# Kernel optimization log

Measured on AMD Instinct MI355X. Metric: run time of the kernel, lower is better.

## Reference

```python
import jax, jax.numpy as jnp
import numpy as np

B, S, W = 16, 256, 128            # batch, seq_len (word pieces), words per sentence
V, H, L, NH, DH, FF, C = 30522, 768, 12, 12, 64, 3072, 425
EPS = 1e-12                        # HF Bert LayerNorm eps


def setup_inputs() -> dict:
    key = jax.random.key(0)
    kiter = iter(jax.random.split(key, 64))
    nk = lambda: next(kiter)
    # each word maps to 1 or 2 word-pieces -> total pieces in [W, 2W] <= S
    word_piece_tracked = jax.random.randint(nk(), (B, W), 1, 3)
    lengths = jnp.sum(word_piece_tracked, axis=1)
    encoded_batch = jax.random.randint(nk(), (B, S), 0, V)
    mask = (jnp.arange(S)[None, :] < lengths[:, None]).astype(jnp.int32)
    p = lambda *shape: jax.random.normal(nk(), shape, jnp.float32) * 0.02
    return dict(
        encoded_batch=encoded_batch, mask=mask, word_piece_tracked=word_piece_tracked,
        word_emb=p(V, H), pos_emb=p(S, H), type_emb=p(1, H),
        emb_ln_s=jnp.ones((H,), jnp.float32), emb_ln_b=jnp.zeros((H,), jnp.float32),
        Wq=p(L, H, H), bq=p(L, H), Wk=p(L, H, H), bk=p(L, H),
        Wv=p(L, H, H), bv=p(L, H), Wo=p(L, H, H), bo=p(L, H),
        ln1_s=jnp.ones((L, H), jnp.float32), ln1_b=jnp.zeros((L, H), jnp.float32),
        Wi=p(L, H, FF), bi=p(L, FF), Wo2=p(L, FF, H), bo2=p(L, H),
        ln2_s=jnp.ones((L, H), jnp.float32), ln2_b=jnp.zeros((L, H), jnp.float32),
        w1=p(H, 1024), b1=p(1024), w2=p(1024, C), b2=p(C),
    )


def _layer_norm(x, s, b):
    mu = jnp.mean(x, -1, keepdims=True)
    var = jnp.var(x, -1, keepdims=True)
    return (x - mu) * jax.lax.rsqrt(var + EPS) * s + b


def _forward(encoded_batch, mask, word_piece_tracked,
             word_emb, pos_emb, type_emb, emb_ln_s, emb_ln_b,
             Wq, bq, Wk, bk, Wv, bv, Wo, bo, ln1_s, ln1_b,
             Wi, bi, Wo2, bo2, ln2_s, ln2_b, w1, b1, w2, b2):
    # BERT embeddings (token_type all zeros)
    x = word_emb[encoded_batch] + pos_emb[None, :, :] + type_emb[0]
    x = _layer_norm(x, emb_ln_s, emb_ln_b)
    attn_bias = (1.0 - mask.astype(jnp.float32))[:, None, None, :] * -10000.0
    scale = 1.0 / np.sqrt(DH).astype(np.float32)

    def step(h, lp):
        wq, bq_, wk, bk_, wv, bv_, wo, bo_, l1s, l1b, wi, bi_, wo2, bo2_, l2s, l2b = lp
        q = (h @ wq + bq_).reshape(B, S, NH, DH)
        k = (h @ wk + bk_).reshape(B, S, NH, DH)
        v = (h @ wv + bv_).reshape(B, S, NH, DH)
        att = jax.nn.softmax(jnp.einsum('bqhd,bkhd->bhqk', q, k) * scale + attn_bias, axis=-1)
        ctx = jnp.einsum('bhqk,bkhd->bqhd', att, v).reshape(B, S, H)
        h = _layer_norm(h + ctx @ wo + bo_, l1s, l1b)
        ff = jax.nn.gelu(h @ wi + bi_, approximate=False)
        h = _layer_norm(h + ff @ wo2 + bo2_, l2s, l2b)
        return h, None

    x, _ = jax.lax.scan(step, x, (Wq, bq, Wk, bk, Wv, bv, Wo, bo, ln1_s, ln1_b,
                                  Wi, bi, Wo2, bo2, ln2_s, ln2_b))

    # MLP head (dropout = identity in eval)
    f1 = jax.nn.relu(x) @ w1 + b1          # [B, S, 1024]
    f2 = jax.nn.relu(f1) @ w2 + b2          # [B, S, C]

    # ragged segment-mean pooling over word pieces (equiv. to the python loop)
    cum = jnp.cumsum(word_piece_tracked, axis=1)                         # [B, W]
    seg = jax.vmap(lambda c: jnp.searchsorted(c, jnp.arange(S), side='right'))(cum)  # [B, S]
    sums = jax.vmap(lambda f, s: jax.ops.segment_sum(f, s, num_segments=W))(f2, seg)
    pooled = sums / word_piece_tracked[..., None].astype(f2.dtype)       # [B, W, C]
    out = jnp.concatenate([pooled, f2[:, W:, :]], axis=1)                # [B, S, C]
    return jax.nn.softmax(out, axis=2)


def reference(encoded_batch, mask, word_piece_tracked,
              word_emb, pos_emb, type_emb, emb_ln_s, emb_ln_b,
              Wq, bq, Wk, bk, Wv, bv, Wo, bo, ln1_s, ln1_b,
              Wi, bi, Wo2, bo2, ln2_s, ln2_b, w1, b1, w2, b2):
    return _forward(encoded_batch, mask, word_piece_tracked,
                    word_emb, pos_emb, type_emb, emb_ln_s, emb_ln_b,
                    Wq, bq, Wk, bk, Wv, bv, Wo, bo, ln1_s, ln1_b,
                    Wi, bi, Wo2, bo2, ln2_s, ln2_b, w1, b1, w2, b2)
```

## Files before the change

### kernel.cpp

```cpp
#include <hip/hip_runtime.h>
#include <math.h>

#define BB 16
#define SS 256
#define WW 128
#define HH 768
#define LL 12
#define NHH 12
#define DHH 64
#define FFD 3072
#define CC 425
#define NTOK (BB*SS)
#define QKVN (3*HH)

typedef __attribute__((ext_vector_type(8))) short bf16x8;
typedef __attribute__((ext_vector_type(4))) float f32x4;

__device__ __forceinline__ float bf2f(unsigned short u) {
    union { unsigned int i; float f; } z; z.i = ((unsigned int)u) << 16; return z.f;
}
__device__ __forceinline__ unsigned short f2bf(float f) {
    union { float f; unsigned int i; } z; z.f = f;
    unsigned int i = z.i;
    unsigned int r = (i + 0x7fffu + ((i >> 16) & 1u)) >> 16;
    return (unsigned short)r;
}

__device__ __forceinline__ void gload16(const void* g, void* l) {
    __builtin_amdgcn_global_load_lds((const __attribute__((address_space(1))) void*)g,
                                     (__attribute__((address_space(3))) void*)l, 16, 0, 0);
}

__device__ __forceinline__ float gelu_f(float v) {
    float ax = fabsf(v) * 0.70710678118654752f;
    float t = 1.0f / fmaf(0.3275911f, ax, 1.0f);
    float poly = t * fmaf(t, fmaf(t, fmaf(t, fmaf(t, 1.061405429f, -1.453152027f),
                                          1.421413741f), -0.284496736f), 0.254829592f);
    float er = 1.0f - poly * __expf(-ax * ax);
    er = (v < 0.f) ? -er : er;
    return 0.5f * v * (1.0f + er);
}

__device__ __forceinline__ int xcd_remap(int nwg, int orig) {
    int q = nwg >> 3, r = nwg & 7, xc = orig & 7, o8 = orig >> 3;
    return (xc < r ? xc * (q + 1) : r * (q + 1) + (xc - r) * q) + o8;
}

template<int ACT_C>
__launch_bounds__(512)
__global__ void gemm128(const unsigned short* __restrict__ A,
                        const unsigned short* __restrict__ Bt,
                        const float* __restrict__ bias,
                        unsigned short* __restrict__ Cm,
                        int M, int N, int K, int ldC) {
    constexpr int BUFS = 128 * 32;
    __shared__ __align__(16) unsigned short lA[2 * BUFS];
    __shared__ __align__(16) unsigned short lB[2 * BUFS];
    const int tid = threadIdx.x, w = tid >> 6, l = tid & 63;

    const int gx = gridDim.x;
    const int wg = xcd_remap(gx * gridDim.y, blockIdx.y * gx + blockIdx.x);
    const int m0 = (wg / gx) * 128, n0 = (wg % gx) * 128;

    const int wr = (w >> 2) * 64, wc = (w & 3) * 32;
    const int lr = l & 15, lk = (l >> 4) * 8;
    const int rsw = ((lr >> 1) & 3) << 4;
    const int lrow = l >> 2;
    const int gs = (l & 3) ^ ((lrow >> 1) & 3);

    f32x4 acc[4][2];
#pragma unroll
    for (int m = 0; m < 4; ++m)
#pragma unroll
        for (int n = 0; n < 2; ++n) acc[m][n] = (f32x4){0.f, 0.f, 0.f, 0.f};

    auto stage = [&](int k0, unsigned short* dA, unsigned short* dB) {
        gload16(A + (size_t)(m0 + w * 16 + lrow) * K + k0 + gs * 8, dA + w * 512);
        gload16(Bt + (size_t)(n0 + w * 16 + lrow) * K + k0 + gs * 8, dB + w * 512);
    };

    const int nt = K >> 5;
    stage(0, lA, lB);
    __syncthreads();

    for (int t = 0; t < nt; ++t) {
        unsigned short* cA = lA + (t & 1) * BUFS;
        unsigned short* cB = lB + (t & 1) * BUFS;
        if (t + 1 < nt)
            stage((t + 1) << 5, lA + ((t + 1) & 1) * BUFS, lB + ((t + 1) & 1) * BUFS);
        bf16x8 af[4], bfr[2];
#pragma unroll
        for (int m = 0; m < 4; ++m) {
            int row = wr + m * 16 + lr;
            af[m] = *(const bf16x8*)((const char*)cA + row * 64 + ((lk * 2) ^ rsw));
        }
#pragma unroll
        for (int n = 0; n < 2; ++n) {
            int row = wc + n * 16 + lr;
            bfr[n] = *(const bf16x8*)((const char*)cB + row * 64 + ((lk * 2) ^ rsw));
        }
#pragma unroll
        for (int m = 0; m < 4; ++m)
#pragma unroll
            for (int n = 0; n < 2; ++n)
                acc[m][n] = __builtin_amdgcn_mfma_f32_16x16x32_bf16(af[m], bfr[n], acc[m][n], 0, 0, 0);
        __syncthreads();
    }

    const int orow = (l >> 4) * 4, ocol = l & 15;
#pragma unroll
    for (int m = 0; m < 4; ++m)
#pragma unroll
        for (int n = 0; n < 2; ++n) {
            int c = n0 + wc + n * 16 + ocol;
            if (c >= N) continue;
            float bb = bias[c];
#pragma unroll
            for (int j = 0; j < 4; ++j) {
                int rr = m0 + wr + m * 16 + orow + j;
                float vv = acc[m][n][j] + bb;
                if (ACT_C == 1) vv = gelu_f(vv);
                if (ACT_C == 2) vv = fmaxf(vv, 0.f);
                Cm[(size_t)rr * ldC + c] = f2bf(vv);
            }
        }
}

template<int ACT_C>
__launch_bounds__(256)
__global__ void gemm64(const unsigned short* __restrict__ A,
                       const unsigned short* __restrict__ Bt,
                       const float* __restrict__ bias,
                       unsigned short* __restrict__ Cm,
                       int M, int N, int K, int ldC) {
    constexpr int BUFS = 2 * 64 * 32;
    __shared__ __align__(16) unsigned short lA[2 * BUFS];
    __shared__ __align__(16) unsigned short lB[2 * BUFS];
    const int tid = threadIdx.x, w = tid >> 6, l = tid & 63;

    const int gx = gridDim.x;
    const int wg = xcd_remap(gx * gridDim.y, blockIdx.y * gx + blockIdx.x);
    const int m0 = (wg / gx) * 64, n0 = (wg % gx) * 64;

    const int wr = (w >> 1) * 32, wc = (w & 1) * 32;
    const int lr = l & 15, lk = (l >> 4) * 8;
    const int rsw = ((lr >> 1) & 3) << 4;
    const int lrow = l >> 2;
    const int gs = (l & 3) ^ ((lrow >> 1) & 3);

    f32x4 acc[2][2];
#pragma unroll
    for (int m = 0; m < 2; ++m)
#pragma unroll
        for (int n = 0; n < 2; ++n) acc[m][n] = (f32x4){0.f, 0.f, 0.f, 0.f};

    auto stage = [&](int k0, unsigned short* dA, unsigned short* dB) {
#pragma unroll
        for (int h = 0; h < 2; ++h) {
            gload16(A + (size_t)(m0 + w * 16 + lrow) * K + k0 + h * 32 + gs * 8,
                    dA + h * 2048 + w * 512);
            gload16(Bt + (size_t)(n0 + w * 16 + lrow) * K + k0 + h * 32 + gs * 8,
                    dB + h * 2048 + w * 512);
        }
    };

    const int nt = K >> 6;
    stage(0, lA, lB);
    __syncthreads();

    for (int t = 0; t < nt; ++t) {
        unsigned short* cA = lA + (t & 1) * BUFS;
        unsigned short* cB = lB + (t & 1) * BUFS;
        if (t + 1 < nt)
            stage((t + 1) << 6, lA + ((t + 1) & 1) * BUFS, lB + ((t + 1) & 1) * BUFS);
#pragma unroll
        for (int h = 0; h < 2; ++h) {
            bf16x8 af[2], bfr[2];
#pragma unroll
            for (int m = 0; m < 2; ++m) {
                int row = wr + m * 16 + lr;
                af[m] = *(const bf16x8*)((const char*)cA + h * 4096 + row * 64 + ((lk * 2) ^ rsw));
            }
#pragma unroll
            for (int n = 0; n < 2; ++n) {
                int row = wc + n * 16 + lr;
                bfr[n] = *(const bf16x8*)((const char*)cB + h * 4096 + row * 64 + ((lk * 2) ^ rsw));
            }
#pragma unroll
            for (int m = 0; m < 2; ++m)
#pragma unroll
                for (int n = 0; n < 2; ++n)
                    acc[m][n] = __builtin_amdgcn_mfma_f32_16x16x32_bf16(af[m], bfr[n], acc[m][n], 0, 0, 0);
        }
        __syncthreads();
    }

    const int orow = (l >> 4) * 4, ocol = l & 15;
#pragma unroll
    for (int m = 0; m < 2; ++m)
#pragma unroll
        for (int n = 0; n < 2; ++n) {
            int c = n0 + wc + n * 16 + ocol;
            if (c >= N) continue;
            float bb = bias[c];
#pragma unroll
            for (int j = 0; j < 4; ++j) {
                int rr = m0 + wr + m * 16 + orow + j;
                float vv = acc[m][n][j] + bb;
                if (ACT_C == 1) vv = gelu_f(vv);
                if (ACT_C == 2) vv = fmaxf(vv, 0.f);
                Cm[(size_t)rr * ldC + c] = f2bf(vv);
            }
        }
}

template<int ACT_A, int ACT_C>
__launch_bounds__(256)
__global__ void gemm_aw(const unsigned short* __restrict__ A,
                        const float* __restrict__ Wm,
                        const float* __restrict__ bias,
                        unsigned short* __restrict__ Cm,
                        int M, int N, int K, int ldC) {
    __shared__ __align__(16) unsigned short lA[64][40];
    __shared__ __align__(16) unsigned short lB[64][40];
    const int tid = threadIdx.x;
    const int m0 = blockIdx.y * 64;
    const int n0 = blockIdx.x * 64;
    const int w = tid >> 6, l = tid & 63;
    const int wr = (w >> 1) * 32, wc = (w & 1) * 32;
    const int lr = l & 15, lk = (l >> 4) * 8;

    f32x4 acc[2][2];
#pragma unroll
    for (int m = 0; m < 2; ++m)
#pragma unroll
        for (int n = 0; n < 2; ++n) acc[m][n] = (f32x4){0.f, 0.f, 0.f, 0.f};

    const int arow = tid >> 2, akc = (tid & 3) << 3;
    const int bkr = tid >> 3, bnc = (tid & 7) << 3;
    const bool nvec = (N & 7) == 0;

    for (int k0 = 0; k0 < K; k0 += 32) {
        uint4 av = *(const uint4*)(A + (size_t)(m0 + arow) * K + (k0 + akc));
        if (ACT_A) {
            unsigned short* p = (unsigned short*)&av;
#pragma unroll
            for (int j = 0; j < 8; ++j) if (p[j] & 0x8000u) p[j] = 0;
        }
        *(uint4*)&lA[arow][akc] = av;
        unsigned short bv[8];
        if (nvec) {
            const float* wp = Wm + (size_t)(k0 + bkr) * N + (n0 + bnc);
            float4 w0 = *(const float4*)(wp);
            float4 w1 = *(const float4*)(wp + 4);
            bv[0] = f2bf(w0.x); bv[1] = f2bf(w0.y); bv[2] = f2bf(w0.z); bv[3] = f2bf(w0.w);
            bv[4] = f2bf(w1.x); bv[5] = f2bf(w1.y); bv[6] = f2bf(w1.z); bv[7] = f2bf(w1.w);
        } else {
#pragma unroll
            for (int j = 0; j < 8; ++j) {
                int col = n0 + bnc + j;
                bv[j] = (col < N) ? f2bf(Wm[(size_t)(k0 + bkr) * N + col]) : (unsigned short)0;
            }
        }
#pragma unroll
        for (int j = 0; j < 8; ++j) lB[bnc + j][bkr] = bv[j];
        __syncthreads();

        bf16x8 af[2], bfr[2];
#pragma unroll
        for (int m = 0; m < 2; ++m) af[m] = *(const bf16x8*)&lA[wr + m * 16 + lr][lk];
#pragma unroll
        for (int n = 0; n < 2; ++n) bfr[n] = *(const bf16x8*)&lB[wc + n * 16 + lr][lk];
#pragma unroll
        for (int m = 0; m < 2; ++m)
#pragma unroll
            for (int n = 0; n < 2; ++n)
                acc[m][n] = __builtin_amdgcn_mfma_f32_16x16x32_bf16(af[m], bfr[n], acc[m][n], 0, 0, 0);
        __syncthreads();
    }

    const int orow = (l >> 4) * 4, ocol = l & 15;
#pragma unroll
    for (int m = 0; m < 2; ++m)
#pragma unroll
        for (int n = 0; n < 2; ++n) {
            int c = n0 + wc + n * 16 + ocol;
            if (c >= N) continue;
            float bb = bias[c];
#pragma unroll
            for (int j = 0; j < 4; ++j) {
                int r = m0 + wr + m * 16 + orow + j;
                float vv = acc[m][n][j] + bb;
                if (ACT_C == 1) vv = gelu_f(vv);
                if (ACT_C == 2) vv = fmaxf(vv, 0.f);
                Cm[(size_t)r * ldC + c] = f2bf(vv);
            }
        }
}

__global__ void transpose_w(const float* __restrict__ src, unsigned short* __restrict__ dst,
                            int K, int N, long srcLS, long dstLS) {
    int n0 = blockIdx.x * 32, k0 = blockIdx.y * 32;
    src += (size_t)blockIdx.z * srcLS;
    dst += (size_t)blockIdx.z * dstLS;
    __shared__ float tile[32][33];
    int tx = threadIdx.x & 31, ty = threadIdx.x >> 5;
#pragma unroll
    for (int r = 0; r < 4; ++r) {
        int k = k0 + ty + r * 8, n = n0 + tx;
        tile[ty + r * 8][tx] = (n < N && k < K) ? src[(size_t)k * N + n] : 0.f;
    }
    __syncthreads();
    int col2 = threadIdx.x & 15, rowb = threadIdx.x >> 4;
#pragma unroll
    for (int p = 0; p < 2; ++p) {
        int n = n0 + rowb + p * 16;
        unsigned int lo = f2bf(tile[col2 * 2][rowb + p * 16]);
        unsigned int hi = f2bf(tile[col2 * 2 + 1][rowb + p * 16]);
        *(unsigned int*)(dst + (size_t)n * K + k0 + col2 * 2) = lo | (hi << 16);
    }
}

__global__ void concat_bias(const float* bq, const float* bk, const float* bv, float* bqkv) {
    int i = blockIdx.x * 256 + threadIdx.x;
    if (i >= LL * QKVN) return;
    int lyr = i / QKVN, c = i % QKVN;
    float v = (c < HH) ? bq[lyr * HH + c] : (c < 2 * HH) ? bk[lyr * HH + c - HH] : bv[lyr * HH + c - 2 * HH];
    bqkv[i] = v;
}

__global__ void build_maskbias(const int* mask, float* mb) {
    int i = blockIdx.x * 256 + threadIdx.x;
    mb[i] = mask[i] ? 0.0f : -10000.0f;
}

__launch_bounds__(256)
__global__ void attention_mfma(const unsigned short* __restrict__ qkv,
                               const float* __restrict__ mb,
                               unsigned short* __restrict__ ctx) {
    const int qt = blockIdx.x, h = blockIdx.y, b = blockIdx.z;
    const int tid = threadIdx.x, w = tid >> 6, l = tid & 63;
    __shared__ __align__(16) unsigned short lK[SS * DHH];
    __shared__ __align__(16) unsigned short lVt[DHH * SS];
    const size_t tokbase = (size_t)b * SS * QKVN;

    {
        const unsigned short* kp = qkv + tokbase + (size_t)tid * QKVN + HH + h * DHH;
        const unsigned short* vp = kp + HH;
#pragma unroll
        for (int c = 0; c < 8; ++c) {
            uint4 kd = *(const uint4*)(kp + c * 8);
            *(uint4*)((char*)lK + ((tid * 128 + c * 16) ^ ((tid & 7) << 4))) = kd;
            uint4 vd = *(const uint4*)(vp + c * 8);
            const unsigned short* e = (const unsigned short*)&vd;
#pragma unroll
            for (int j = 0; j < 8; ++j) {
                int d = c * 8 + j;
                *(unsigned short*)((char*)lVt + ((d * 512 + tid * 2) ^ ((d & 7) << 4))) = e[j];
            }
        }
    }
    const int q0w = qt * 64 + w * 16;
    const unsigned short* qp = qkv + tokbase + (size_t)(q0w + (l & 15)) * QKVN + h * DHH + (l >> 4) * 8;
    bf16x8 aq0 = *(const bf16x8*)(qp);
    bf16x8 aq1 = *(const bf16x8*)(qp + 32);
    __syncthreads();

    f32x4 sc[16];
#pragma unroll
    for (int t = 0; t < 16; ++t) {
        int key = t * 16 + (l & 15);
        int base = key * 128;
        int sw = (key & 7) << 4;
        bf16x8 bk0 = *(const bf16x8*)((char*)lK + ((base + (l >> 4) * 16) ^ sw));
        bf16x8 bk1 = *(const bf16x8*)((char*)lK + ((base + 64 + (l >> 4) * 16) ^ sw));
        f32x4 a = (f32x4){0.f, 0.f, 0.f, 0.f};
        a = __builtin_amdgcn_mfma_f32_16x16x32_bf16(aq0, bk0, a, 0, 0, 0);
        a = __builtin_amdgcn_mfma_f32_16x16x32_bf16(aq1, bk1, a, 0, 0, 0);
        sc[t] = a;
    }
    const float* mbb = mb + b * SS;
    float mx[4] = {-3.0e38f, -3.0e38f, -3.0e38f, -3.0e38f};
#pragma unroll
    for (int t = 0; t < 16; ++t) {
        float mv = mbb[t * 16 + (l & 15)];
#pragma unroll
        for (int r = 0; r < 4; ++r) {
            float v = sc[t][r] * 0.125f + mv;
            sc[t][r] = v;
            mx[r] = fmaxf(mx[r], v);
        }
    }
#pragma unroll
    for (int m = 1; m <= 8; m <<= 1)
#pragma unroll
        for (int r = 0; r < 4; ++r) mx[r] = fmaxf(mx[r], __shfl_xor(mx[r], m));
    float sm[4] = {0.f, 0.f, 0.f, 0.f};
#pragma unroll
    for (int t = 0; t < 16; ++t)
#pragma unroll
        for (int r = 0; r < 4; ++r) {
            float e = __expf(sc[t][r] - mx[r]);
            sc[t][r] = e;
            sm[r] += e;
        }
#pragma unroll
    for (int m = 1; m <= 8; m <<= 1)
#pragma unroll
        for (int r = 0; r < 4; ++r) sm[r] += __shfl_xor(sm[r], m);
    float inv[4];
#pragma unroll
    for (int r = 0; r < 4; ++r) inv[r] = 1.0f / sm[r];

    __syncthreads();
    unsigned short* P = lK;
#pragma unroll
    for (int t = 0; t < 16; ++t)
#pragma unroll
        for (int r = 0; r < 4; ++r) {
            int prow = w * 16 + (l >> 4) * 4 + r;
            int pcol = t * 16 + (l & 15);
            *(unsigned short*)((char*)P + ((prow * 512 + pcol * 2) ^ ((prow & 7) << 4))) =
                f2bf(sc[t][r] * inv[r]);
        }
    __syncthreads();

    f32x4 o[4];
#pragma unroll
    for (int dt = 0; dt < 4; ++dt) o[dt] = (f32x4){0.f, 0.f, 0.f, 0.f};
#pragma unroll
    for (int kt = 0; kt < 8; ++kt) {
        int prow = w * 16 + (l & 15);
        int pkb = (kt * 32 + (l >> 4) * 8) * 2;
        bf16x8 pa = *(const bf16x8*)((char*)P + ((prow * 512 + pkb) ^ ((prow & 7) << 4)));
#pragma unroll
        for (int dt = 0; dt < 4; ++dt) {
            int d = dt * 16 + (l & 15);
            bf16x8 vb = *(const bf16x8*)((char*)lVt + ((d * 512 + pkb) ^ ((d & 7) << 4)));
            o[dt] = __builtin_amdgcn_mfma_f32_16x16x32_bf16(pa, vb, o[dt], 0, 0, 0);
        }
    }
#pragma unroll
    for (int dt = 0; dt < 4; ++dt)
#pragma unroll
        for (int r = 0; r < 4; ++r) {
            int q = qt * 64 + w * 16 + (l >> 4) * 4 + r;
            int d = dt * 16 + (l & 15);
            ctx[((size_t)(b * SS + q)) * HH + h * DHH + d] = f2bf(o[dt][r]);
        }
}

__global__ void embed_ln(const int* __restrict__ ids,
                         const float* __restrict__ we,
                         const float* __restrict__ pe,
                         const float* __restrict__ te,
                         const float* __restrict__ g,
                         const float* __restrict__ beta,
                         unsigned short* __restrict__ x) {
    int t = blockIdx.x, s = t % SS, tid = threadIdx.x;
    int id = ids[t];
    __shared__ float r1[256], r2[256];
    float e[3]; float sum = 0.f, sq = 0.f;
#pragma unroll
    for (int j = 0; j < 3; ++j) {
        int i = tid + j * 256;
        float v = we[(size_t)id * HH + i] + pe[(size_t)s * HH + i] + te[i];
        e[j] = v; sum += v; sq += v * v;
    }
    r1[tid] = sum; r2[tid] = sq; __syncthreads();
    for (int o = 128; o > 0; o >>= 1) {
        if (tid < o) { r1[tid] += r1[tid + o]; r2[tid] += r2[tid + o]; }
        __syncthreads();
    }
    float mu = r1[0] * (1.0f / HH);
    float var = fmaxf(r2[0] * (1.0f / HH) - mu * mu, 0.f);
    float rs = rsqrtf(var + 1e-12f);
#pragma unroll
    for (int j = 0; j < 3; ++j) {
        int i = tid + j * 256;
        x[(size_t)t * HH + i] = f2bf((e[j] - mu) * rs * g[i] + beta[i]);
    }
}

template<int WRITE_RELU>
__launch_bounds__(256)
__global__ void add_ln(unsigned short* __restrict__ x,
                       const unsigned short* __restrict__ y,
                       const float* __restrict__ g,
                       const float* __restrict__ beta,
                       unsigned short* __restrict__ xr) {
    const int t = blockIdx.x * 4 + (threadIdx.x >> 6);
    const int l = threadIdx.x & 63;
    const size_t base = (size_t)t * HH;
    float v[12];
    float sum = 0.f, sq = 0.f;
#pragma unroll
    for (int j = 0; j < 3; ++j) {
        uint2 xa = *(const uint2*)(x + base + j * 256 + l * 4);
        uint2 ya = *(const uint2*)(y + base + j * 256 + l * 4);
        const unsigned short* xp = (const unsigned short*)&xa;
        const unsigned short* yp = (const unsigned short*)&ya;
#pragma unroll
        for (int e = 0; e < 4; ++e) {
            float vv = bf2f(xp[e]) + bf2f(yp[e]);
            v[j * 4 + e] = vv;
            sum += vv; sq += vv * vv;
        }
    }
#pragma unroll
    for (int m = 1; m < 64; m <<= 1) {
        sum += __shfl_xor(sum, m);
        sq += __shfl_xor(sq, m);
    }
    float mu = sum * (1.0f / HH);
    float var = fmaxf(sq * (1.0f / HH) - mu * mu, 0.f);
    float rs = rsqrtf(var + 1e-12f);
#pragma unroll
    for (int j = 0; j < 3; ++j) {
        float4 gg = *(const float4*)(g + j * 256 + l * 4);
        float4 bb = *(const float4*)(beta + j * 256 + l * 4);
        float r0 = (v[j * 4 + 0] - mu) * rs * gg.x + bb.x;
        float r1 = (v[j * 4 + 1] - mu) * rs * gg.y + bb.y;
        float r2 = (v[j * 4 + 2] - mu) * rs * gg.z + bb.z;
        float r3 = (v[j * 4 + 3] - mu) * rs * gg.w + bb.w;
        uint2 st = {(unsigned)f2bf(r0) | ((unsigned)f2bf(r1) << 16),
                    (unsigned)f2bf(r2) | ((unsigned)f2bf(r3) << 16)};
        *(uint2*)(x + base + j * 256 + l * 4) = st;
        if (WRITE_RELU) {
            uint2 sr = {(unsigned)f2bf(fmaxf(r0, 0.f)) | ((unsigned)f2bf(fmaxf(r1, 0.f)) << 16),
                        (unsigned)f2bf(fmaxf(r2, 0.f)) | ((unsigned)f2bf(fmaxf(r3, 0.f)) << 16)};
            *(uint2*)(xr + base + j * 256 + l * 4) = sr;
        }
    }
}

__global__ void cumsum_k(const int* __restrict__ wpt, int* __restrict__ cum) {
    int b = blockIdx.x, w = threadIdx.x;
    int s = 0;
    for (int j = 0; j <= w; ++j) s += wpt[b * WW + j];
    cum[b * WW + w] = s;
}

__global__ void pool_softmax(const unsigned short* __restrict__ f2,
                             const int* __restrict__ cum,
                             float* __restrict__ out) {
    int t = blockIdx.x, b = t / SS, s = t % SS, tid = threadIdx.x;
    __shared__ float red[512];
    float val = -1e30f;
    bool act = tid < CC;
    if (act) {
        if (s < WW) {
            int end = cum[b * WW + s];
            int start = s ? cum[b * WW + s - 1] : 0;
            float su = 0.f;
            for (int j = start; j < end; ++j) su += bf2f(f2[((size_t)b * SS + j) * CC + tid]);
            val = su / (float)(end - start);
        } else {
            val = bf2f(f2[((size_t)b * SS + s) * CC + tid]);
        }
    }
    red[tid] = val; __syncthreads();
    for (int o = 256; o > 0; o >>= 1) {
        if (tid < o) red[tid] = fmaxf(red[tid], red[tid + o]);
        __syncthreads();
    }
    float mx = red[0]; __syncthreads();
    float e = act ? expf(val - mx) : 0.f;
    red[tid] = e; __syncthreads();
    for (int o = 256; o > 0; o >>= 1) {
        if (tid < o) red[tid] += red[tid + o];
        __syncthreads();
    }
    float inv = 1.0f / red[0];
    if (act) out[((size_t)b * SS + s) * CC + tid] = e * inv;
}

static inline size_t al256(size_t x) { return (x + 255) & ~(size_t)255; }

extern "C" void kernel_launch(void* const* d_in, const int* in_sizes, int n_in,
                              void* d_out, int out_size, void* d_ws, size_t ws_size,
                              hipStream_t stream) {
    const int* enc   = (const int*)d_in[0];
    const int* mask  = (const int*)d_in[1];
    const int* wpt   = (const int*)d_in[2];
    const float* word_emb = (const float*)d_in[3];
    const float* pos_emb  = (const float*)d_in[4];
    const float* type_emb = (const float*)d_in[5];
    const float* eln_s = (const float*)d_in[6];
    const float* eln_b = (const float*)d_in[7];
    const float* Wq = (const float*)d_in[8];
    const float* bq = (const float*)d_in[9];
    const float* Wk = (const float*)d_in[10];
    const float* bk = (const float*)d_in[11];
    const float* Wv = (const float*)d_in[12];
    const float* bv = (const float*)d_in[13];
    const float* Wo = (const float*)d_in[14];
    const float* bo = (const float*)d_in[15];
    const float* ln1s = (const float*)d_in[16];
    const float* ln1b = (const float*)d_in[17];
    const float* Wi = (const float*)d_in[18];
    const float* bi = (const float*)d_in[19];
    const float* Wo2 = (const float*)d_in[20];
    const float* bo2 = (const float*)d_in[21];
    const float* ln2s = (const float*)d_in[22];
    const float* ln2b = (const float*)d_in[23];
    const float* w1 = (const float*)d_in[24];
    const float* b1 = (const float*)d_in[25];
    const float* w2 = (const float*)d_in[26];
    const float* b2 = (const float*)d_in[27];

    unsigned char* ws = (unsigned char*)d_ws;
    size_t off = 0;
    unsigned short* x    = (unsigned short*)(ws + off); off = al256(off + (size_t)NTOK * HH * 2);
    unsigned short* qkv  = (unsigned short*)(ws + off); off = al256(off + (size_t)NTOK * QKVN * 2);
    unsigned short* ctx  = (unsigned short*)(ws + off); off = al256(off + (size_t)NTOK * HH * 2);
    unsigned short* proj = (unsigned short*)(ws + off); off = al256(off + (size_t)NTOK * HH * 2);
    unsigned short* ff   = (unsigned short*)(ws + off); off = al256(off + (size_t)NTOK * FFD * 2);
    unsigned short* f1   = (unsigned short*)(ws + off); off = al256(off + (size_t)NTOK * 1024 * 2);
    unsigned short* f2   = (unsigned short*)(ws + off); off = al256(off + (size_t)NTOK * CC * 2);
    unsigned short* xr   = (unsigned short*)(ws + off); off = al256(off + (size_t)NTOK * HH * 2);
    float* mb            = (float*)(ws + off);          off = al256(off + (size_t)NTOK * 4);
    int* cum             = (int*)(ws + off);            off = al256(off + (size_t)BB * WW * 4);
    float* bqkv          = (float*)(ws + off);          off = al256(off + (size_t)LL * QKVN * 4);
    size_t offFast = off;
    unsigned short* WqkvT = (unsigned short*)(ws + offFast); offFast = al256(offFast + (size_t)LL * QKVN * HH * 2);
    unsigned short* WoT   = (unsigned short*)(ws + offFast); offFast = al256(offFast + (size_t)LL * HH * HH * 2);
    unsigned short* WiT   = (unsigned short*)(ws + offFast); offFast = al256(offFast + (size_t)LL * FFD * HH * 2);
    unsigned short* Wo2T  = (unsigned short*)(ws + offFast); offFast = al256(offFast + (size_t)LL * HH * FFD * 2);
    unsigned short* w1T   = (unsigned short*)(ws + offFast); offFast = al256(offFast + (size_t)1024 * HH * 2);
    unsigned short* w2T   = (unsigned short*)(ws + offFast); offFast = al256(offFast + (size_t)512 * 1024 * 2);
    const bool fast = (ws_size >= offFast);

    build_maskbias<<<NTOK / 256, 256, 0, stream>>>(mask, mb);
    concat_bias<<<(LL * QKVN + 255) / 256, 256, 0, stream>>>(bq, bk, bv, bqkv);

    if (fast) {
        transpose_w<<<dim3(24, 24, LL), 256, 0, stream>>>(Wq, WqkvT, HH, HH, (long)HH * HH, (long)QKVN * HH);
        transpose_w<<<dim3(24, 24, LL), 256, 0, stream>>>(Wk, WqkvT + (size_t)HH * HH, HH, HH, (long)HH * HH, (long)QKVN * HH);
        transpose_w<<<dim3(24, 24, LL), 256, 0, stream>>>(Wv, WqkvT + (size_t)2 * HH * HH, HH, HH, (long)HH * HH, (long)QKVN * HH);
        transpose_w<<<dim3(24, 24, LL), 256, 0, stream>>>(Wo, WoT, HH, HH, (long)HH * HH, (long)HH * HH);
        transpose_w<<<dim3(96, 24, LL), 256, 0, stream>>>(Wi, WiT, HH, FFD, (long)HH * FFD, (long)FFD * HH);
        transpose_w<<<dim3(24, 96, LL), 256, 0, stream>>>(Wo2, Wo2T, FFD, HH, (long)FFD * HH, (long)HH * FFD);
        transpose_w<<<dim3(32, 24, 1), 256, 0, stream>>>(w1, w1T, HH, 1024, 0, 0);
        transpose_w<<<dim3(16, 32, 1), 256, 0, stream>>>(w2, w2T, 1024, CC, 0, 0);
    }

    embed_ln<<<NTOK, 256, 0, stream>>>(enc, word_emb, pos_emb, type_emb, eln_s, eln_b, x);

    const dim3 gQKV(QKVN / 128, NTOK / 128);
    const dim3 gWo(HH / 64, NTOK / 64);
    const dim3 gFF1(FFD / 128, NTOK / 128);
    const dim3 gFF2(HH / 64, NTOK / 64);
    const dim3 gH1(1024 / 64, NTOK / 64);
    const dim3 gH2(7, NTOK / 64);
    const dim3 gAttn(4, NHH, BB);

    for (int l = 0; l < LL; ++l) {
        if (fast) {
            gemm128<0><<<gQKV, 512, 0, stream>>>(x, WqkvT + (size_t)l * QKVN * HH, bqkv + l * QKVN, qkv, NTOK, QKVN, HH, QKVN);
        } else {
            const dim3 g64(HH / 64, NTOK / 64);
            gemm_aw<0, 0><<<g64, 256, 0, stream>>>(x, Wq + (size_t)l * HH * HH, bq + l * HH, qkv, NTOK, HH, HH, QKVN);
            gemm_aw<0, 0><<<g64, 256, 0, stream>>>(x, Wk + (size_t)l * HH * HH, bk + l * HH, qkv + HH, NTOK, HH, HH, QKVN);
            gemm_aw<0, 0><<<g64, 256, 0, stream>>>(x, Wv + (size_t)l * HH * HH, bv + l * HH, qkv + 2 * HH, NTOK, HH, HH, QKVN);
        }
        attention_mfma<<<gAttn, 256, 0, stream>>>(qkv, mb, ctx);
        if (fast) {
            gemm64<0><<<gWo, 256, 0, stream>>>(ctx, WoT + (size_t)l * HH * HH, bo + l * HH, proj, NTOK, HH, HH, HH);
        } else {
            gemm_aw<0, 0><<<dim3(HH / 64, NTOK / 64), 256, 0, stream>>>(ctx, Wo + (size_t)l * HH * HH, bo + l * HH, proj, NTOK, HH, HH, HH);
        }
        add_ln<0><<<NTOK / 4, 256, 0, stream>>>(x, proj, ln1s + l * HH, ln1b + l * HH, nullptr);
        if (fast) {
            gemm128<1><<<gFF1, 512, 0, stream>>>(x, WiT + (size_t)l * FFD * HH, bi + l * FFD, ff, NTOK, FFD, HH, FFD);
            gemm64<0><<<gFF2, 256, 0, stream>>>(ff, Wo2T + (size_t)l * HH * FFD, bo2 + l * HH, proj, NTOK, HH, FFD, HH);
        } else {
            gemm_aw<0, 1><<<dim3(FFD / 64, NTOK / 64), 256, 0, stream>>>(x, Wi + (size_t)l * HH * FFD, bi + l * FFD, ff, NTOK, FFD, HH, FFD);
            gemm_aw<0, 0><<<dim3(HH / 64, NTOK / 64), 256, 0, stream>>>(ff, Wo2 + (size_t)l * FFD * HH, bo2 + l * HH, proj, NTOK, HH, FFD, HH);
        }
        if (l == LL - 1)
            add_ln<1><<<NTOK / 4, 256, 0, stream>>>(x, proj, ln2s + l * HH, ln2b + l * HH, xr);
        else
            add_ln<0><<<NTOK / 4, 256, 0, stream>>>(x, proj, ln2s + l * HH, ln2b + l * HH, nullptr);
    }

    if (fast) {
        gemm64<2><<<gH1, 256, 0, stream>>>(xr, w1T, b1, f1, NTOK, 1024, HH, 1024);
        gemm64<0><<<gH2, 256, 0, stream>>>(f1, w2T, b2, f2, NTOK, CC, 1024, CC);
    } else {
        gemm_aw<0, 2><<<dim3(1024 / 64, NTOK / 64), 256, 0, stream>>>(xr, w1, b1, f1, NTOK, 1024, HH, 1024);
        gemm_aw<0, 0><<<dim3(7, NTOK / 64), 256, 0, stream>>>(f1, w2, b2, f2, NTOK, CC, 1024, CC);
    }
    cumsum_k<<<BB, WW, 0, stream>>>(wpt, cum);
    pool_softmax<<<NTOK, 512, 0, stream>>>(f2, cum, (float*)d_out);
}
```

Before: 1.997 ms.

## Split-K the FFN down-projection GEMM and reorder prefetch with MFMA priority

Replaces the FF2 GEMM (K=3072, N=768) with a two-way split-K kernel that writes fp32 partials into the reused qkv buffer, followed by a combine kernel that adds the partials and bias and converts to bf16. This doubles the workgroup count for a GEMM with a small output tile grid and long K, at the cost of extra fp32 partial traffic and one more launch per layer. Separately, the 128-tile GEMM now issues the next-stage global loads after reading its LDS fragments and raises wave priority around the MFMA block. The aim is better overlap of loads with matrix math.

```diff
diff --git a/kernel.cpp b/kernel.cpp
--- a/kernel.cpp
+++ b/kernel.cpp
@@ -86,8 +86,6 @@
     for (int t = 0; t < nt; ++t) {
         unsigned short* cA = lA + (t & 1) * BUFS;
         unsigned short* cB = lB + (t & 1) * BUFS;
-        if (t + 1 < nt)
-            stage((t + 1) << 5, lA + ((t + 1) & 1) * BUFS, lB + ((t + 1) & 1) * BUFS);
         bf16x8 af[4], bfr[2];
 #pragma unroll
         for (int m = 0; m < 4; ++m) {
@@ -99,11 +97,15 @@
             int row = wc + n * 16 + lr;
             bfr[n] = *(const bf16x8*)((const char*)cB + row * 64 + ((lk * 2) ^ rsw));
         }
+        if (t + 1 < nt)
+            stage((t + 1) << 5, lA + ((t + 1) & 1) * BUFS, lB + ((t + 1) & 1) * BUFS);
+        __builtin_amdgcn_s_setprio(1);
 #pragma unroll
         for (int m = 0; m < 4; ++m)
 #pragma unroll
             for (int n = 0; n < 2; ++n)
                 acc[m][n] = __builtin_amdgcn_mfma_f32_16x16x32_bf16(af[m], bfr[n], acc[m][n], 0, 0, 0);
+        __builtin_amdgcn_s_setprio(0);
         __syncthreads();
     }
 
@@ -212,6 +214,107 @@
                 Cm[(size_t)rr * ldC + c] = f2bf(vv);
             }
         }
+}
+
+template<int NS>
+__launch_bounds__(256)
+__global__ void gemm64sk(const unsigned short* __restrict__ A,
+                         const unsigned short* __restrict__ Bt,
+                         float* __restrict__ P,
+                         int M, int N, int K) {
+    constexpr int BUFS = 2 * 64 * 32;
+    __shared__ __align__(16) unsigned short lA[2 * BUFS];
+    __shared__ __align__(16) unsigned short lB[2 * BUFS];
+    const int tid = threadIdx.x, w = tid >> 6, l = tid & 63;
+    const int z = blockIdx.z;
+    const int Kc = K / NS;
+    A += z * Kc;
+    Bt += z * Kc;
+    P += (size_t)z * M * N;
+
+    const int gx = gridDim.x;
+    const int wg = xcd_remap(gx * gridDim.y, blockIdx.y * gx + blockIdx.x);
+    const int m0 = (wg / gx) * 64, n0 = (wg % gx) * 64;
+
+    const int wr = (w >> 1) * 32, wc = (w & 1) * 32;
+    const int lr = l & 15, lk = (l >> 4) * 8;
+    const int rsw = ((lr >> 1) & 3) << 4;
+    const int lrow = l >> 2;
+    const int gs = (l & 3) ^ ((lrow >> 1) & 3);
+
+    f32x4 acc[2][2];
+#pragma unroll
+    for (int m = 0; m < 2; ++m)
+#pragma unroll
+        for (int n = 0; n < 2; ++n) acc[m][n] = (f32x4){0.f, 0.f, 0.f, 0.f};
+
+    auto stage = [&](int k0, unsigned short* dA, unsigned short* dB) {
+#pragma unroll
+        for (int h = 0; h < 2; ++h) {
+            gload16(A + (size_t)(m0 + w * 16 + lrow) * K + k0 + h * 32 + gs * 8,
+                    dA + h * 2048 + w * 512);
+            gload16(Bt + (size_t)(n0 + w * 16 + lrow) * K + k0 + h * 32 + gs * 8,
+                    dB + h * 2048 + w * 512);
+        }
+    };
+
+    const int nt = Kc >> 6;
+    stage(0, lA, lB);
+    __syncthreads();
+
+    for (int t = 0; t < nt; ++t) {
+        unsigned short* cA = lA + (t & 1) * BUFS;
+        unsigned short* cB = lB + (t & 1) * BUFS;
+        if (t + 1 < nt)
+            stage((t + 1) << 6, lA + ((t + 1) & 1) * BUFS, lB + ((t + 1) & 1) * BUFS);
+#pragma unroll
+        for (int h = 0; h < 2; ++h) {
+            bf16x8 af[2], bfr[2];
+#pragma unroll
+            for (int m = 0; m < 2; ++m) {
+                int row = wr + m * 16 + lr;
+                af[m] = *(const bf16x8*)((const char*)cA + h * 4096 + row * 64 + ((lk * 2) ^ rsw));
+            }
+#pragma unroll
+            for (int n = 0; n < 2; ++n) {
+                int row = wc + n * 16 + lr;
+                bfr[n] = *(const bf16x8*)((const char*)cB + h * 4096 + row * 64 + ((lk * 2) ^ rsw));
+            }
+#pragma unroll
+            for (int m = 0; m < 2; ++m)
+#pragma unroll
+                for (int n = 0; n < 2; ++n)
+                    acc[m][n] = __builtin_amdgcn_mfma_f32_16x16x32_bf16(af[m], bfr[n], acc[m][n], 0, 0, 0);
+        }
+        __syncthreads();
+    }
+
+    const int orow = (l >> 4) * 4, ocol = l & 15;
+#pragma unroll
+    for (int m = 0; m < 2; ++m)
+#pragma unroll
+        for (int n = 0; n < 2; ++n) {
+            int c = n0 + wc + n * 16 + ocol;
+#pragma unroll
+            for (int j = 0; j < 4; ++j) {
+                int rr = m0 + wr + m * 16 + orow + j;
+                P[(size_t)rr * N + c] = acc[m][n][j];
+            }
+        }
+}
+
+__global__ void combine2(const float* __restrict__ P, const float* __restrict__ bias,
+                         unsigned short* __restrict__ C, int MN, int N) {
+    int i = blockIdx.x * 256 + threadIdx.x;
+    if (i * 4 >= MN) return;
+    float4 a = ((const float4*)P)[i];
+    float4 b = ((const float4*)(P + MN))[i];
+    int c = (i * 4) % N;
+    float4 bs = *(const float4*)(bias + c);
+    unsigned int o0 = f2bf(a.x + b.x + bs.x) | ((unsigned)f2bf(a.y + b.y + bs.y) << 16);
+    unsigned int o1 = f2bf(a.z + b.z + bs.z) | ((unsigned)f2bf(a.w + b.w + bs.w) << 16);
+    uint2 st = {o0, o1};
+    *(uint2*)(C + (size_t)i * 4) = st;
 }
 
 template<int ACT_A, int ACT_C>
@@ -622,6 +725,7 @@
     float* mb            = (float*)(ws + off);          off = al256(off + (size_t)NTOK * 4);
     int* cum             = (int*)(ws + off);            off = al256(off + (size_t)BB * WW * 4);
     float* bqkv          = (float*)(ws + off);          off = al256(off + (size_t)LL * QKVN * 4);
+    float* Psplit = (float*)qkv;
     size_t offFast = off;
     unsigned short* WqkvT = (unsigned short*)(ws + offFast); offFast = al256(offFast + (size_t)LL * QKVN * HH * 2);
     unsigned short* WoT   = (unsigned short*)(ws + offFast); offFast = al256(offFast + (size_t)LL * HH * HH * 2);
@@ -650,7 +754,7 @@
     const dim3 gQKV(QKVN / 128, NTOK / 128);
     const dim3 gWo(HH / 64, NTOK / 64);
     const dim3 gFF1(FFD / 128, NTOK / 128);
-    const dim3 gFF2(HH / 64, NTOK / 64);
+    const dim3 gFF2(HH / 64, NTOK / 64, 2);
     const dim3 gH1(1024 / 64, NTOK / 64);
     const dim3 gH2(7, NTOK / 64);
     const dim3 gAttn(4, NHH, BB);
@@ -673,7 +777,8 @@
         add_ln<0><<<NTOK / 4, 256, 0, stream>>>(x, proj, ln1s + l * HH, ln1b + l * HH, nullptr);
         if (fast) {
             gemm128<1><<<gFF1, 512, 0, stream>>>(x, WiT + (size_t)l * FFD * HH, bi + l * FFD, ff, NTOK, FFD, HH, FFD);
-            gemm64<0><<<gFF2, 256, 0, stream>>>(ff, Wo2T + (size_t)l * HH * FFD, bo2 + l * HH, proj, NTOK, HH, FFD, HH);
+            gemm64sk<2><<<gFF2, 256, 0, stream>>>(ff, Wo2T + (size_t)l * HH * FFD, Psplit, NTOK, HH, FFD);
+            combine2<<<(NTOK * HH / 4 + 255) / 256, 256, 0, stream>>>(Psplit, bo2 + l * HH, proj, NTOK * HH, HH);
         } else {
             gemm_aw<0, 1><<<dim3(FFD / 64, NTOK / 64), 256, 0, stream>>>(x, Wi + (size_t)l * HH * FFD, bi + l * FFD, ff, NTOK, FFD, HH, FFD);
             gemm_aw<0, 0><<<dim3(HH / 64, NTOK / 64), 256, 0, stream>>>(ff, Wo2 + (size_t)l * FFD * HH, bo2 + l * HH, proj, NTOK, HH, FFD, HH);
```

Result: slower. 2.037 ms (+2.0%).
